# Kernel tuning notes

Measured on AMD Instinct MI355X. Metric: run time of the kernel, lower is better.

Reference implementation:

```python
import jax, jax.numpy as jnp
import numpy as np

B, NT, NZ, NX, NREC = 4, 256, 192, 192, 128
DT, DH = 0.001, 10.0


def setup_inputs() -> dict:
    key = jax.random.key(0)
    k1, k2, k3, k4 = jax.random.split(key, 4)
    # source wavelets, one trace per shot
    x = jax.random.normal(k1, (B, NT, 1), dtype=jnp.float32) * 1e2
    # realistic elastic media
    vp = 2500.0 + 1000.0 * jax.random.uniform(k2, (NZ, NX), dtype=jnp.float32)
    vs = vp / 1.78
    rho = 2000.0 + 300.0 * jax.random.uniform(k3, (NZ, NX), dtype=jnp.float32)
    # per-shot source location (z=5 near surface, random x)
    src_x = jax.random.randint(k4, (B,), 10, NX - 10)
    src_loc = jnp.stack([jnp.full((B,), 5), src_x], axis=1).astype(jnp.int32)
    # receiver line at depth z=5
    rec_x = jnp.linspace(10, NX - 10, NREC).astype(jnp.int32)
    rec_loc = jnp.stack([jnp.full((NREC,), 5, dtype=jnp.int32), rec_x], axis=1)
    return {"x": x, "vp": vp, "vs": vs, "rho": rho,
            "src_loc": src_loc, "rec_loc": rec_loc}


# staggered-grid first differences (forward / backward), zero-padded at edges
def _dxf(f):
    return jnp.pad(jnp.diff(f, axis=-1), ((0, 0), (0, 0), (0, 1))) / DH

def _dxb(f):
    return jnp.pad(jnp.diff(f, axis=-1), ((0, 0), (0, 0), (1, 0))) / DH

def _dzf(f):
    return jnp.pad(jnp.diff(f, axis=-2), ((0, 0), (0, 1), (0, 0))) / DH

def _dzb(f):
    return jnp.pad(jnp.diff(f, axis=-2), ((0, 0), (1, 0), (0, 0))) / DH


def _propagate(x, vp, vs, rho, src_loc, rec_loc):
    lam = rho * (vp ** 2 - 2.0 * vs ** 2)
    mu = rho * vs ** 2
    lam2mu = lam + 2.0 * mu
    buoy = DT / rho  # buoyancy * dt
    bidx = jnp.arange(B)
    sz, sx = src_loc[:, 0], src_loc[:, 1]
    rz, rx = rec_loc[:, 0], rec_loc[:, 1]

    def step(carry, wav_t):
        vx, vz, txx, tzz, txz = carry
        # velocity update from stress divergence
        vx = vx + buoy * (_dxf(txx) + _dzb(txz))
        vz = vz + buoy * (_dxb(txz) + _dzf(tzz))
        # stress update from velocity gradients
        dvxdx = _dxb(vx)
        dvzdz = _dzb(vz)
        txx = txx + DT * (lam2mu * dvxdx + lam * dvzdz)
        tzz = tzz + DT * (lam * dvxdx + lam2mu * dvzdz)
        txz = txz + DT * mu * (_dzf(vx) + _dxf(vz))
        # explosive source injection into txx, tzz (source_type = ['txx','tzz'])
        txx = txx.at[bidx, sz, sx].add(wav_t)
        tzz = tzz.at[bidx, sz, sx].add(wav_t)
        # probe extraction: (B, NREC)
        return (vx, vz, txx, tzz, txz), (vx[:, rz, rx], vz[:, rz, rx])

    z = jnp.zeros((B, NZ, NX), dtype=vp.dtype)
    _, (rvx, rvz) = jax.lax.scan(step, (z, z, z, z, z), x[:, :, 0].T)
    # torch: stack(dim=1) -> (B,NT,NREC); permute(1,2,0) -> (NT,NREC,B); cat dim=2
    y_vx = jnp.transpose(rvx, (0, 2, 1))  # (NT, NREC, B)
    y_vz = jnp.transpose(rvz, (0, 2, 1))
    return jnp.concatenate([y_vx, y_vz], axis=2)  # (NT, NREC, 2B)


def reference(x, vp, vs, rho, src_loc, rec_loc):
    return _propagate(x, vp, vs, rho, src_loc, rec_loc)
```

## Files before the change

### kernel.cpp

```cpp
#include <hip/hip_runtime.h>

#pragma clang fp contract(off)

#define B_    4
#define NT_   256
#define NZ_   192
#define NX_   192
#define NREC_ 128
#define DT_   0.001f
#define DH_   10.0f

#define N_CELL  (NZ_ * NX_)
#define N_FIELD (B_ * N_CELL)

#define K_     4
#define ROWS   3
#define NTHR   1024
#define VH     (2 * K_ - 1)
#define SH     (2 * K_)
#define VROWS  (ROWS + 2 * VH)
#define SROWS  (ROWS + 2 * SH)
#define TILES  (NZ_ / ROWS)
#define NBLK   (B_ * TILES)
#define NX4    (NX_ / 4)
#define LDS_BYTES ((2 * VROWS + 3 * SROWS) * NX_ * 4)

using f4 = __attribute__((ext_vector_type(4))) float;

__device__ __forceinline__ int imax_(int a, int b) { return a > b ? a : b; }
__device__ __forceinline__ int imin_(int a, int b) { return a < b ? a : b; }

__global__ void mat_kernel(const float* __restrict__ vp, const float* __restrict__ vs,
                           const float* __restrict__ rho,
                           float* __restrict__ lam, float* __restrict__ dtmu,
                           float* __restrict__ lam2mu, float* __restrict__ buoy) {
    int i = blockIdx.x * blockDim.x + threadIdx.x;
    if (i >= N_CELL) return;
    float vpi = vp[i], vsi = vs[i], rhoi = rho[i];
    float vs2 = vsi * vsi;
    float mui = rhoi * vs2;
    float lami = rhoi * (vpi * vpi - 2.0f * vs2);
    lam[i] = lami;
    dtmu[i] = DT_ * mui;
    lam2mu[i] = lami + 2.0f * mui;
    buoy[i] = DT_ / rhoi;
}

template<int S>
__device__ __forceinline__ void substep(
    int tid, int z0, int base, int zv0, int zs0, int sz, int sx, int b, int t0,
    float* __restrict__ vxl, float* __restrict__ vzl,
    float* __restrict__ txxl, float* __restrict__ tzzl, float* __restrict__ txzl,
    const float* __restrict__ lam, const float* __restrict__ dtmu,
    const float* __restrict__ l2m, const float* __restrict__ buoy,
    const float* __restrict__ wav,
    bool rec_ok, int rec_idx, float* __restrict__ out,
    float* __restrict__ vxw, float* __restrict__ vzw,
    float* __restrict__ txxw, float* __restrict__ tzzw, float* __restrict__ txzw) {
    const int t = t0 + S;

    {
        constexpr int hv = 2 * (K_ - 1 - S) + 1;
        const int zlo = imax_(0, z0 - hv);
        const int zhi = imin_(NZ_ - 1, z0 + ROWS - 1 + hv);
        const int n4  = (zhi - zlo + 1) * NX4;
        if (tid < n4) {
            int dz = tid / NX4;
            int x4 = tid - dz * NX4;
            int z  = zlo + dz;
            int x0 = x4 * 4;
            int zsrow = (z - zs0) * NX_;
            int zvrow = (z - zv0) * NX_;
            const f4* txxR = reinterpret_cast<const f4*>(txxl + zsrow);
            const f4* txzR = reinterpret_cast<const f4*>(txzl + zsrow);
            const f4* txzM = reinterpret_cast<const f4*>(txzl + zsrow - NX_);
            const f4* tzzR = reinterpret_cast<const f4*>(tzzl + zsrow);
            const f4* tzzP = reinterpret_cast<const f4*>(tzzl + zsrow + NX_);
            f4 txo  = txxR[x4];
            f4 txn  = txxR[x4 < NX4 - 1 ? x4 + 1 : x4];
            f4 tzo  = txzR[x4];
            f4 tzp  = txzR[x4 > 0 ? x4 - 1 : x4];
            f4 tzm  = txzM[x4];
            f4 tzzo = tzzR[x4];
            f4 tzzp = tzzP[x4];
            f4 vxo  = reinterpret_cast<const f4*>(vxl + zvrow)[x4];
            f4 vzo  = reinterpret_cast<const f4*>(vzl + zvrow)[x4];
            f4 bu   = *reinterpret_cast<const f4*>(buoy + z * NX_ + x0);
            f4 nvx, nvz;
#pragma unroll
            for (int e = 0; e < 4; ++e) {
                int xg = x0 + e;
                float txx_c = txo[e];
                float txxp1 = (e == 3) ? txn[0] : txo[e + 1];
                float txz_c = tzo[e];
                float txzm1 = (e == 0) ? tzp[3] : tzo[e - 1];
                float dxf_txx = (xg < NX_ - 1) ? (txxp1 - txx_c) / DH_ : 0.0f;
                float dzb_txz = (z >= 1)       ? (txz_c - tzm[e]) / DH_ : 0.0f;
                float dxb_txz = (xg >= 1)      ? (txz_c - txzm1) / DH_ : 0.0f;
                float dzf_tzz = (z < NZ_ - 1)  ? (tzzp[e] - tzzo[e]) / DH_ : 0.0f;
                nvx[e] = vxo[e] + bu[e] * (dxf_txx + dzb_txz);
                nvz[e] = vzo[e] + bu[e] * (dxb_txz + dzf_tzz);
            }
            reinterpret_cast<f4*>(vxl + zvrow)[x4] = nvx;
            reinterpret_cast<f4*>(vzl + zvrow)[x4] = nvz;
            if (S == K_ - 1) {
                if (z >= z0 && z < z0 + ROWS) {
                    *reinterpret_cast<f4*>(vxw + base + z * NX_ + x0) = nvx;
                    *reinterpret_cast<f4*>(vzw + base + z * NX_ + x0) = nvz;
                }
            }
        }
    }
    __syncthreads();

    if (rec_ok) {
        size_t o = ((size_t)t * NREC_ + tid) * (2 * B_);
        out[o + b]      = vxl[rec_idx];
        out[o + B_ + b] = vzl[rec_idx];
    }

    {
        constexpr int hs = 2 * (K_ - 1 - S);
        const int zlo = imax_(0, z0 - hs);
        const int zhi = imin_(NZ_ - 1, z0 + ROWS - 1 + hs);
        const int n4  = (zhi - zlo + 1) * NX4;
        if (tid < n4) {
            int dz = tid / NX4;
            int x4 = tid - dz * NX4;
            int z  = zlo + dz;
            int x0 = x4 * 4;
            int zsrow = (z - zs0) * NX_;
            int zvrow = (z - zv0) * NX_;
            const f4* vxR = reinterpret_cast<const f4*>(vxl + zvrow);
            const f4* vxP = reinterpret_cast<const f4*>(vxl + zvrow + NX_);
            const f4* vzR = reinterpret_cast<const f4*>(vzl + zvrow);
            const f4* vzM = reinterpret_cast<const f4*>(vzl + zvrow - NX_);
            f4 vxo  = vxR[x4];
            f4 vxp  = vxR[x4 > 0 ? x4 - 1 : x4];
            f4 vxzp = vxP[x4];
            f4 vzo  = vzR[x4];
            f4 vzn  = vzR[x4 < NX4 - 1 ? x4 + 1 : x4];
            f4 vzm  = vzM[x4];
            f4 txxo = reinterpret_cast<const f4*>(txxl + zsrow)[x4];
            f4 tzzo = reinterpret_cast<const f4*>(tzzl + zsrow)[x4];
            f4 txzo = reinterpret_cast<const f4*>(txzl + zsrow)[x4];
            int c0 = z * NX_ + x0;
            f4 l   = *reinterpret_cast<const f4*>(lam  + c0);
            f4 lm  = *reinterpret_cast<const f4*>(l2m  + c0);
            f4 dtm = *reinterpret_cast<const f4*>(dtmu + c0);
            float w = wav[b * NT_ + t];
            f4 ntxx, ntzz, ntxz;
#pragma unroll
            for (int e = 0; e < 4; ++e) {
                int xg = x0 + e;
                float vx_c = vxo[e];
                float vz_c = vzo[e];
                float vxm1 = (e == 0) ? vxp[3] : vxo[e - 1];
                float vzp1 = (e == 3) ? vzn[0] : vzo[e + 1];
                float dvxdx  = (xg >= 1)      ? (vx_c - vxm1) / DH_ : 0.0f;
                float dvzdz  = (z >= 1)       ? (vz_c - vzm[e]) / DH_ : 0.0f;
                float dzf_vx = (z < NZ_ - 1)  ? (vxzp[e] - vx_c) / DH_ : 0.0f;
                float dxf_vz = (xg < NX_ - 1) ? (vzp1 - vz_c) / DH_ : 0.0f;
                float a  = txxo[e] + DT_ * (lm[e] * dvxdx + l[e] * dvzdz);
                float bb = tzzo[e] + DT_ * (l[e] * dvxdx + lm[e] * dvzdz);
                float cc = txzo[e] + dtm[e] * (dzf_vx + dxf_vz);
                if (z == sz && xg == sx) { a = a + w; bb = bb + w; }
                ntxx[e] = a; ntzz[e] = bb; ntxz[e] = cc;
            }
            reinterpret_cast<f4*>(txxl + zsrow)[x4] = ntxx;
            reinterpret_cast<f4*>(tzzl + zsrow)[x4] = ntzz;
            reinterpret_cast<f4*>(txzl + zsrow)[x4] = ntxz;
            if (S == K_ - 1) {
                *reinterpret_cast<f4*>(txxw + base + c0) = ntxx;
                *reinterpret_cast<f4*>(tzzw + base + c0) = ntzz;
                *reinterpret_cast<f4*>(txzw + base + c0) = ntxz;
            }
        }
    }
    __syncthreads();
}

__global__ void __launch_bounds__(NTHR, 4)
step_kernel(const float* __restrict__ vxr, const float* __restrict__ vzr,
            const float* __restrict__ txxr, const float* __restrict__ tzzr,
            const float* __restrict__ txzr,
            float* __restrict__ vxw, float* __restrict__ vzw,
            float* __restrict__ txxw, float* __restrict__ tzzw, float* __restrict__ txzw,
            const float* __restrict__ lam, const float* __restrict__ dtmu,
            const float* __restrict__ l2m, const float* __restrict__ buoy,
            const float* __restrict__ wav, int t0,
            const int* __restrict__ src_loc, const int* __restrict__ rec_loc,
            float* __restrict__ out) {
    extern __shared__ float smem[];
    float* __restrict__ vxl  = smem;
    float* __restrict__ vzl  = vxl  + VROWS * NX_;
    float* __restrict__ txxl = vzl  + VROWS * NX_;
    float* __restrict__ tzzl = txxl + SROWS * NX_;
    float* __restrict__ txzl = tzzl + SROWS * NX_;

    const int tid  = threadIdx.x;
    const int b    = blockIdx.x / TILES;
    const int tile = blockIdx.x % TILES;
    const int z0   = tile * ROWS;
    const int base = b * N_CELL;
    const int zv0  = z0 - VH;
    const int zs0  = z0 - SH;

    const int sz = src_loc[2 * b];
    const int sx = src_loc[2 * b + 1];

    bool rec_ok = false;
    int rec_idx = 0;
    if (tid < NREC_) {
        int rz = rec_loc[2 * tid];
        int rx = rec_loc[2 * tid + 1];
        if (rz >= z0 && rz < z0 + ROWS) {
            rec_ok = true;
            rec_idx = (rz - zv0) * NX_ + rx;
        }
    }

    if (tid < SROWS * NX4) {
        int dz = tid / NX4;
        int x4 = tid - dz * NX4;
        int z  = zs0 + dz;
        if (z >= 0 && z < NZ_) {
            int g = base + z * NX_ + x4 * 4;
            reinterpret_cast<f4*>(txxl)[tid] = *reinterpret_cast<const f4*>(txxr + g);
            reinterpret_cast<f4*>(tzzl)[tid] = *reinterpret_cast<const f4*>(tzzr + g);
            reinterpret_cast<f4*>(txzl)[tid] = *reinterpret_cast<const f4*>(txzr + g);
        }
    }
    if (tid < VROWS * NX4) {
        int dz = tid / NX4;
        int x4 = tid - dz * NX4;
        int z  = zv0 + dz;
        if (z >= 0 && z < NZ_) {
            int g = base + z * NX_ + x4 * 4;
            reinterpret_cast<f4*>(vxl)[tid] = *reinterpret_cast<const f4*>(vxr + g);
            reinterpret_cast<f4*>(vzl)[tid] = *reinterpret_cast<const f4*>(vzr + g);
        }
    }
    __syncthreads();

    substep<0>(tid, z0, base, zv0, zs0, sz, sx, b, t0, vxl, vzl, txxl, tzzl, txzl,
               lam, dtmu, l2m, buoy, wav, rec_ok, rec_idx, out, vxw, vzw, txxw, tzzw, txzw);
    substep<1>(tid, z0, base, zv0, zs0, sz, sx, b, t0, vxl, vzl, txxl, tzzl, txzl,
               lam, dtmu, l2m, buoy, wav, rec_ok, rec_idx, out, vxw, vzw, txxw, tzzw, txzw);
    substep<2>(tid, z0, base, zv0, zs0, sz, sx, b, t0, vxl, vzl, txxl, tzzl, txzl,
               lam, dtmu, l2m, buoy, wav, rec_ok, rec_idx, out, vxw, vzw, txxw, tzzw, txzw);
    substep<3>(tid, z0, base, zv0, zs0, sz, sx, b, t0, vxl, vzl, txxl, tzzl, txzl,
               lam, dtmu, l2m, buoy, wav, rec_ok, rec_idx, out, vxw, vzw, txxw, tzzw, txzw);
}

extern "C" void kernel_launch(void* const* d_in, const int* in_sizes, int n_in,
                              void* d_out, int out_size, void* d_ws, size_t ws_size,
                              hipStream_t stream) {
    const float* xw      = (const float*)d_in[0];
    const float* vp      = (const float*)d_in[1];
    const float* vs      = (const float*)d_in[2];
    const float* rho     = (const float*)d_in[3];
    const int*   src_loc = (const int*)d_in[4];
    const int*   rec_loc = (const int*)d_in[5];
    float*       out     = (float*)d_out;

    float* ws = (float*)d_ws;
    float* vx[2]  = { ws + 0 * N_FIELD, ws + 1 * N_FIELD };
    float* vz[2]  = { ws + 2 * N_FIELD, ws + 3 * N_FIELD };
    float* txx[2] = { ws + 4 * N_FIELD, ws + 5 * N_FIELD };
    float* tzz[2] = { ws + 6 * N_FIELD, ws + 7 * N_FIELD };
    float* txz[2] = { ws + 8 * N_FIELD, ws + 9 * N_FIELD };
    float* lam    = ws + 10 * N_FIELD;
    float* dtmu   = lam + N_CELL;
    float* l2m    = dtmu + N_CELL;
    float* buoy   = l2m + N_CELL;

    hipMemsetAsync(d_ws, 0, (size_t)10 * N_FIELD * sizeof(float), stream);

    mat_kernel<<<(N_CELL + 255) / 256, 256, 0, stream>>>(vp, vs, rho, lam, dtmu, l2m, buoy);

    for (int L = 0; L < NT_ / K_; ++L) {
        int p = L & 1;
        step_kernel<<<NBLK, NTHR, LDS_BYTES, stream>>>(
            vx[p], vz[p], txx[p], tzz[p], txz[p],
            vx[1 - p], vz[1 - p], txx[1 - p], tzz[1 - p], txz[1 - p],
            lam, dtmu, l2m, buoy,
            xw, L * K_, src_loc, rec_loc, out);
    }
}
```

Before: 1.198 ms.

## Deepen temporal blocking to eight steps, load first substep from global, remap XCDs

Raises temporal blocking from four to eight time steps per launch, which halves the number of kernel launches and global round-trips while enlarging the redundant halo recomputation (the halo now exceeds the thread count, so the work is looped). The separate global-to-LDS prologue is removed: substep 0 reads its stencil inputs straight from global memory, and the LDS stress halo shrinks accordingly. Block indices are remapped across 8 XCDs so neighbouring tiles share an L2, and the occupancy hint in the launch bounds is dropped. The cost is more LDS per block, more halo compute and fewer resident blocks.

```diff
diff --git a/kernel.cpp b/kernel.cpp
--- a/kernel.cpp
+++ b/kernel.cpp
@@ -13,22 +13,25 @@
 #define N_CELL  (NZ_ * NX_)
 #define N_FIELD (B_ * N_CELL)
 
-#define K_     4
+#define K_     8
 #define ROWS   3
 #define NTHR   1024
 #define VH     (2 * K_ - 1)
-#define SH     (2 * K_)
+#define HS0    (2 * (K_ - 1))
 #define VROWS  (ROWS + 2 * VH)
-#define SROWS  (ROWS + 2 * SH)
+#define SROWSL (ROWS + 2 * HS0)
 #define TILES  (NZ_ / ROWS)
 #define NBLK   (B_ * TILES)
 #define NX4    (NX_ / 4)
-#define LDS_BYTES ((2 * VROWS + 3 * SROWS) * NX_ * 4)
+#define NXCD   8
+#define LDS_BYTES ((2 * VROWS + 3 * SROWSL) * NX_ * 4)
 
 using f4 = __attribute__((ext_vector_type(4))) float;
 
 __device__ __forceinline__ int imax_(int a, int b) { return a > b ? a : b; }
 __device__ __forceinline__ int imin_(int a, int b) { return a < b ? a : b; }
+__device__ __forceinline__ f4 LD4(const float* p) { return *reinterpret_cast<const f4*>(p); }
+__device__ __forceinline__ void ST4(float* p, f4 v) { *reinterpret_cast<f4*>(p) = v; }
 
 __global__ void mat_kernel(const float* __restrict__ vp, const float* __restrict__ vs,
                            const float* __restrict__ rho,
@@ -51,6 +54,9 @@
     int tid, int z0, int base, int zv0, int zs0, int sz, int sx, int b, int t0,
     float* __restrict__ vxl, float* __restrict__ vzl,
     float* __restrict__ txxl, float* __restrict__ tzzl, float* __restrict__ txzl,
+    const float* __restrict__ vxr, const float* __restrict__ vzr,
+    const float* __restrict__ txxr, const float* __restrict__ tzzr,
+    const float* __restrict__ txzr,
     const float* __restrict__ lam, const float* __restrict__ dtmu,
     const float* __restrict__ l2m, const float* __restrict__ buoy,
     const float* __restrict__ wav,
@@ -60,53 +66,71 @@
     const int t = t0 + S;
 
     {
-        constexpr int hv = 2 * (K_ - 1 - S) + 1;
+        constexpr int hv   = 2 * (K_ - 1 - S) + 1;
+        constexpr int MAXR = ROWS + 2 * hv;
+        constexpr int ITER = (MAXR * NX4 + NTHR - 1) / NTHR;
         const int zlo = imax_(0, z0 - hv);
         const int zhi = imin_(NZ_ - 1, z0 + ROWS - 1 + hv);
         const int n4  = (zhi - zlo + 1) * NX4;
-        if (tid < n4) {
-            int dz = tid / NX4;
-            int x4 = tid - dz * NX4;
-            int z  = zlo + dz;
-            int x0 = x4 * 4;
-            int zsrow = (z - zs0) * NX_;
-            int zvrow = (z - zv0) * NX_;
-            const f4* txxR = reinterpret_cast<const f4*>(txxl + zsrow);
-            const f4* txzR = reinterpret_cast<const f4*>(txzl + zsrow);
-            const f4* txzM = reinterpret_cast<const f4*>(txzl + zsrow - NX_);
-            const f4* tzzR = reinterpret_cast<const f4*>(tzzl + zsrow);
-            const f4* tzzP = reinterpret_cast<const f4*>(tzzl + zsrow + NX_);
-            f4 txo  = txxR[x4];
-            f4 txn  = txxR[x4 < NX4 - 1 ? x4 + 1 : x4];
-            f4 tzo  = txzR[x4];
-            f4 tzp  = txzR[x4 > 0 ? x4 - 1 : x4];
-            f4 tzm  = txzM[x4];
-            f4 tzzo = tzzR[x4];
-            f4 tzzp = tzzP[x4];
-            f4 vxo  = reinterpret_cast<const f4*>(vxl + zvrow)[x4];
-            f4 vzo  = reinterpret_cast<const f4*>(vzl + zvrow)[x4];
-            f4 bu   = *reinterpret_cast<const f4*>(buoy + z * NX_ + x0);
-            f4 nvx, nvz;
 #pragma unroll
-            for (int e = 0; e < 4; ++e) {
-                int xg = x0 + e;
-                float txx_c = txo[e];
-                float txxp1 = (e == 3) ? txn[0] : txo[e + 1];
-                float txz_c = tzo[e];
-                float txzm1 = (e == 0) ? tzp[3] : tzo[e - 1];
-                float dxf_txx = (xg < NX_ - 1) ? (txxp1 - txx_c) / DH_ : 0.0f;
-                float dzb_txz = (z >= 1)       ? (txz_c - tzm[e]) / DH_ : 0.0f;
-                float dxb_txz = (xg >= 1)      ? (txz_c - txzm1) / DH_ : 0.0f;
-                float dzf_tzz = (z < NZ_ - 1)  ? (tzzp[e] - tzzo[e]) / DH_ : 0.0f;
-                nvx[e] = vxo[e] + bu[e] * (dxf_txx + dzb_txz);
-                nvz[e] = vzo[e] + bu[e] * (dxb_txz + dzf_tzz);
-            }
-            reinterpret_cast<f4*>(vxl + zvrow)[x4] = nvx;
-            reinterpret_cast<f4*>(vzl + zvrow)[x4] = nvz;
-            if (S == K_ - 1) {
-                if (z >= z0 && z < z0 + ROWS) {
-                    *reinterpret_cast<f4*>(vxw + base + z * NX_ + x0) = nvx;
-                    *reinterpret_cast<f4*>(vzw + base + z * NX_ + x0) = nvz;
+        for (int it = 0; it < ITER; ++it) {
+            int idx = tid + it * NTHR;
+            if (idx < n4) {
+                int dz  = idx / NX4;
+                int x4i = idx - dz * NX4;
+                int x0i = x4i * 4;
+                int z   = zlo + dz;
+                f4 txo, txn, tzo, tzp, tzm, tzzo, tzzp, vxo, vzo;
+                if (S == 0) {
+                    int gz  = base + z * NX_ + x0i;
+                    int gzm = base + imax_(z - 1, 0) * NX_ + x0i;
+                    int gzp = base + imin_(z + 1, NZ_ - 1) * NX_ + x0i;
+                    txo  = LD4(txxr + gz);
+                    txn  = LD4(txxr + gz + (x4i < NX4 - 1 ? 4 : 0));
+                    tzo  = LD4(txzr + gz);
+                    tzp  = LD4(txzr + gz - (x4i > 0 ? 4 : 0));
+                    tzm  = LD4(txzr + gzm);
+                    tzzo = LD4(tzzr + gz);
+                    tzzp = LD4(tzzr + gzp);
+                    vxo  = LD4(vxr + gz);
+                    vzo  = LD4(vzr + gz);
+                } else {
+                    int sOff = (z - zs0) * NX_ + x0i;
+                    int vOff = (z - zv0) * NX_ + x0i;
+                    txo  = LD4(txxl + sOff);
+                    txn  = LD4(txxl + sOff + (x4i < NX4 - 1 ? 4 : 0));
+                    tzo  = LD4(txzl + sOff);
+                    tzp  = LD4(txzl + sOff - (x4i > 0 ? 4 : 0));
+                    tzm  = LD4(txzl + sOff - NX_);
+                    tzzo = LD4(tzzl + sOff);
+                    tzzp = LD4(tzzl + sOff + NX_);
+                    vxo  = LD4(vxl + vOff);
+                    vzo  = LD4(vzl + vOff);
+                }
+                f4 bu = LD4(buoy + z * NX_ + x0i);
+                f4 nvx, nvz;
+#pragma unroll
+                for (int e = 0; e < 4; ++e) {
+                    int xg = x0i + e;
+                    float txx_c = txo[e];
+                    float txxp1 = (e == 3) ? txn[0] : txo[e + 1];
+                    float txz_c = tzo[e];
+                    float txzm1 = (e == 0) ? tzp[3] : tzo[e - 1];
+                    float dxf_txx = (xg < NX_ - 1) ? (txxp1 - txx_c) / DH_ : 0.0f;
+                    float dzb_txz = (z >= 1)       ? (txz_c - tzm[e]) / DH_ : 0.0f;
+                    float dxb_txz = (xg >= 1)      ? (txz_c - txzm1) / DH_ : 0.0f;
+                    float dzf_tzz = (z < NZ_ - 1)  ? (tzzp[e] - tzzo[e]) / DH_ : 0.0f;
+                    nvx[e] = vxo[e] + bu[e] * (dxf_txx + dzb_txz);
+                    nvz[e] = vzo[e] + bu[e] * (dxb_txz + dzf_tzz);
+                }
+                int vOff = (z - zv0) * NX_ + x0i;
+                ST4(vxl + vOff, nvx);
+                ST4(vzl + vOff, nvz);
+                if (S == K_ - 1) {
+                    if (z >= z0 && z < z0 + ROWS) {
+                        ST4(vxw + base + z * NX_ + x0i, nvx);
+                        ST4(vzw + base + z * NX_ + x0i, nvz);
+                    }
                 }
             }
         }
@@ -120,67 +144,79 @@
     }
 
     {
-        constexpr int hs = 2 * (K_ - 1 - S);
+        constexpr int hs   = 2 * (K_ - 1 - S);
+        constexpr int MAXR = ROWS + 2 * hs;
+        constexpr int ITER = (MAXR * NX4 + NTHR - 1) / NTHR;
         const int zlo = imax_(0, z0 - hs);
         const int zhi = imin_(NZ_ - 1, z0 + ROWS - 1 + hs);
         const int n4  = (zhi - zlo + 1) * NX4;
-        if (tid < n4) {
-            int dz = tid / NX4;
-            int x4 = tid - dz * NX4;
-            int z  = zlo + dz;
-            int x0 = x4 * 4;
-            int zsrow = (z - zs0) * NX_;
-            int zvrow = (z - zv0) * NX_;
-            const f4* vxR = reinterpret_cast<const f4*>(vxl + zvrow);
-            const f4* vxP = reinterpret_cast<const f4*>(vxl + zvrow + NX_);
-            const f4* vzR = reinterpret_cast<const f4*>(vzl + zvrow);
-            const f4* vzM = reinterpret_cast<const f4*>(vzl + zvrow - NX_);
-            f4 vxo  = vxR[x4];
-            f4 vxp  = vxR[x4 > 0 ? x4 - 1 : x4];
-            f4 vxzp = vxP[x4];
-            f4 vzo  = vzR[x4];
-            f4 vzn  = vzR[x4 < NX4 - 1 ? x4 + 1 : x4];
-            f4 vzm  = vzM[x4];
-            f4 txxo = reinterpret_cast<const f4*>(txxl + zsrow)[x4];
-            f4 tzzo = reinterpret_cast<const f4*>(tzzl + zsrow)[x4];
-            f4 txzo = reinterpret_cast<const f4*>(txzl + zsrow)[x4];
-            int c0 = z * NX_ + x0;
-            f4 l   = *reinterpret_cast<const f4*>(lam  + c0);
-            f4 lm  = *reinterpret_cast<const f4*>(l2m  + c0);
-            f4 dtm = *reinterpret_cast<const f4*>(dtmu + c0);
-            float w = wav[b * NT_ + t];
-            f4 ntxx, ntzz, ntxz;
 #pragma unroll
-            for (int e = 0; e < 4; ++e) {
-                int xg = x0 + e;
-                float vx_c = vxo[e];
-                float vz_c = vzo[e];
-                float vxm1 = (e == 0) ? vxp[3] : vxo[e - 1];
-                float vzp1 = (e == 3) ? vzn[0] : vzo[e + 1];
-                float dvxdx  = (xg >= 1)      ? (vx_c - vxm1) / DH_ : 0.0f;
-                float dvzdz  = (z >= 1)       ? (vz_c - vzm[e]) / DH_ : 0.0f;
-                float dzf_vx = (z < NZ_ - 1)  ? (vxzp[e] - vx_c) / DH_ : 0.0f;
-                float dxf_vz = (xg < NX_ - 1) ? (vzp1 - vz_c) / DH_ : 0.0f;
-                float a  = txxo[e] + DT_ * (lm[e] * dvxdx + l[e] * dvzdz);
-                float bb = tzzo[e] + DT_ * (l[e] * dvxdx + lm[e] * dvzdz);
-                float cc = txzo[e] + dtm[e] * (dzf_vx + dxf_vz);
-                if (z == sz && xg == sx) { a = a + w; bb = bb + w; }
-                ntxx[e] = a; ntzz[e] = bb; ntxz[e] = cc;
-            }
-            reinterpret_cast<f4*>(txxl + zsrow)[x4] = ntxx;
-            reinterpret_cast<f4*>(tzzl + zsrow)[x4] = ntzz;
-            reinterpret_cast<f4*>(txzl + zsrow)[x4] = ntxz;
-            if (S == K_ - 1) {
-                *reinterpret_cast<f4*>(txxw + base + c0) = ntxx;
-                *reinterpret_cast<f4*>(tzzw + base + c0) = ntzz;
-                *reinterpret_cast<f4*>(txzw + base + c0) = ntxz;
+        for (int it = 0; it < ITER; ++it) {
+            int idx = tid + it * NTHR;
+            if (idx < n4) {
+                int dz  = idx / NX4;
+                int x4i = idx - dz * NX4;
+                int x0i = x4i * 4;
+                int z   = zlo + dz;
+                int vOff = (z - zv0) * NX_ + x0i;
+                f4 vxo  = LD4(vxl + vOff);
+                f4 vxp  = LD4(vxl + vOff - (x4i > 0 ? 4 : 0));
+                f4 vxzp = LD4(vxl + vOff + NX_);
+                f4 vzo  = LD4(vzl + vOff);
+                f4 vzn  = LD4(vzl + vOff + (x4i < NX4 - 1 ? 4 : 0));
+                f4 vzm  = LD4(vzl + vOff - NX_);
+                f4 txxo, tzzo, txzo;
+                if (S == 0) {
+                    int gz = base + z * NX_ + x0i;
+                    txxo = LD4(txxr + gz);
+                    tzzo = LD4(tzzr + gz);
+                    txzo = LD4(txzr + gz);
+                } else {
+                    int sOff = (z - zs0) * NX_ + x0i;
+                    txxo = LD4(txxl + sOff);
+                    tzzo = LD4(tzzl + sOff);
+                    txzo = LD4(txzl + sOff);
+                }
+                int c0 = z * NX_ + x0i;
+                f4 l   = LD4(lam  + c0);
+                f4 lm  = LD4(l2m  + c0);
+                f4 dtm = LD4(dtmu + c0);
+                float w = wav[b * NT_ + t];
+                f4 ntxx, ntzz, ntxz;
+#pragma unroll
+                for (int e = 0; e < 4; ++e) {
+                    int xg = x0i + e;
+                    float vx_c = vxo[e];
+                    float vz_c = vzo[e];
+                    float vxm1 = (e == 0) ? vxp[3] : vxo[e - 1];
+                    float vzp1 = (e == 3) ? vzn[0] : vzo[e + 1];
+                    float dvxdx  = (xg >= 1)      ? (vx_c - vxm1) / DH_ : 0.0f;
+                    float dvzdz  = (z >= 1)       ? (vz_c - vzm[e]) / DH_ : 0.0f;
+                    float dzf_vx = (z < NZ_ - 1)  ? (vxzp[e] - vx_c) / DH_ : 0.0f;
+                    float dxf_vz = (xg < NX_ - 1) ? (vzp1 - vz_c) / DH_ : 0.0f;
+                    float a  = txxo[e] + DT_ * (lm[e] * dvxdx + l[e] * dvzdz);
+                    float bb = tzzo[e] + DT_ * (l[e] * dvxdx + lm[e] * dvzdz);
+                    float cc = txzo[e] + dtm[e] * (dzf_vx + dxf_vz);
+                    if (z == sz && xg == sx) { a = a + w; bb = bb + w; }
+                    ntxx[e] = a; ntzz[e] = bb; ntxz[e] = cc;
+                }
+                int sOff = (z - zs0) * NX_ + x0i;
+                ST4(txxl + sOff, ntxx);
+                ST4(tzzl + sOff, ntzz);
+                ST4(txzl + sOff, ntxz);
+                if (S == K_ - 1) {
+                    int g = base + c0;
+                    ST4(txxw + g, ntxx);
+                    ST4(tzzw + g, ntzz);
+                    ST4(txzw + g, ntxz);
+                }
             }
         }
     }
     __syncthreads();
 }
 
-__global__ void __launch_bounds__(NTHR, 4)
+__global__ void __launch_bounds__(NTHR)
 step_kernel(const float* __restrict__ vxr, const float* __restrict__ vzr,
             const float* __restrict__ txxr, const float* __restrict__ tzzr,
             const float* __restrict__ txzr,
@@ -195,16 +231,17 @@
     float* __restrict__ vxl  = smem;
     float* __restrict__ vzl  = vxl  + VROWS * NX_;
     float* __restrict__ txxl = vzl  + VROWS * NX_;
-    float* __restrict__ tzzl = txxl + SROWS * NX_;
-    float* __restrict__ txzl = tzzl + SROWS * NX_;
+    float* __restrict__ tzzl = txxl + SROWSL * NX_;
+    float* __restrict__ txzl = tzzl + SROWSL * NX_;
 
     const int tid  = threadIdx.x;
-    const int b    = blockIdx.x / TILES;
-    const int tile = blockIdx.x % TILES;
+    const int wg   = (blockIdx.x % NXCD) * (NBLK / NXCD) + blockIdx.x / NXCD;
+    const int b    = wg / TILES;
+    const int tile = wg % TILES;
     const int z0   = tile * ROWS;
     const int base = b * N_CELL;
     const int zv0  = z0 - VH;
-    const int zs0  = z0 - SH;
+    const int zs0  = z0 - HS0;
 
     const int sz = src_loc[2 * b];
     const int sx = src_loc[2 * b + 1];
@@ -220,37 +257,30 @@
         }
     }
 
-    if (tid < SROWS * NX4) {
-        int dz = tid / NX4;
-        int x4 = tid - dz * NX4;
-        int z  = zs0 + dz;
-        if (z >= 0 && z < NZ_) {
-            int g = base + z * NX_ + x4 * 4;
-            reinterpret_cast<f4*>(txxl)[tid] = *reinterpret_cast<const f4*>(txxr + g);
-            reinterpret_cast<f4*>(tzzl)[tid] = *reinterpret_cast<const f4*>(tzzr + g);
-            reinterpret_cast<f4*>(txzl)[tid] = *reinterpret_cast<const f4*>(txzr + g);
-        }
-    }
-    if (tid < VROWS * NX4) {
-        int dz = tid / NX4;
-        int x4 = tid - dz * NX4;
-        int z  = zv0 + dz;
-        if (z >= 0 && z < NZ_) {
-            int g = base + z * NX_ + x4 * 4;
-            reinterpret_cast<f4*>(vxl)[tid] = *reinterpret_cast<const f4*>(vxr + g);
-            reinterpret_cast<f4*>(vzl)[tid] = *reinterpret_cast<const f4*>(vzr + g);
-        }
-    }
-    __syncthreads();
-
     substep<0>(tid, z0, base, zv0, zs0, sz, sx, b, t0, vxl, vzl, txxl, tzzl, txzl,
-               lam, dtmu, l2m, buoy, wav, rec_ok, rec_idx, out, vxw, vzw, txxw, tzzw, txzw);
+               vxr, vzr, txxr, tzzr, txzr, lam, dtmu, l2m, buoy, wav,
+               rec_ok, rec_idx, out, vxw, vzw, txxw, tzzw, txzw);
     substep<1>(tid, z0, base, zv0, zs0, sz, sx, b, t0, vxl, vzl, txxl, tzzl, txzl,
-               lam, dtmu, l2m, buoy, wav, rec_ok, rec_idx, out, vxw, vzw, txxw, tzzw, txzw);
+               vxr, vzr, txxr, tzzr, txzr, lam, dtmu, l2m, buoy, wav,
+               rec_ok, rec_idx, out, vxw, vzw, txxw, tzzw, txzw);
     substep<2>(tid, z0, base, zv0, zs0, sz, sx, b, t0, vxl, vzl, txxl, tzzl, txzl,
-               lam, dtmu, l2m, buoy, wav, rec_ok, rec_idx, out, vxw, vzw, txxw, tzzw, txzw);
+               vxr, vzr, txxr, tzzr, txzr, lam, dtmu, l2m, buoy, wav,
+               rec_ok, rec_idx, out, vxw, vzw, txxw, tzzw, txzw);
     substep<3>(tid, z0, base, zv0, zs0, sz, sx, b, t0, vxl, vzl, txxl, tzzl, txzl,
-               lam, dtmu, l2m, buoy, wav, rec_ok, rec_idx, out, vxw, vzw, txxw, tzzw, txzw);
+               vxr, vzr, txxr, tzzr, txzr, lam, dtmu, l2m, buoy, wav,
+               rec_ok, rec_idx, out, vxw, vzw, txxw, tzzw, txzw);
+    substep<4>(tid, z0, base, zv0, zs0, sz, sx, b, t0, vxl, vzl, txxl, tzzl, txzl,
+               vxr, vzr, txxr, tzzr, txzr, lam, dtmu, l2m, buoy, wav,
+               rec_ok, rec_idx, out, vxw, vzw, txxw, tzzw, txzw);
+    substep<5>(tid, z0, base, zv0, zs0, sz, sx, b, t0, vxl, vzl, txxl, tzzl, txzl,
+               vxr, vzr, txxr, tzzr, txzr, lam, dtmu, l2m, buoy, wav,
+               rec_ok, rec_idx, out, vxw, vzw, txxw, tzzw, txzw);
+    substep<6>(tid, z0, base, zv0, zs0, sz, sx, b, t0, vxl, vzl, txxl, tzzl, txzl,
+               vxr, vzr, txxr, tzzr, txzr, lam, dtmu, l2m, buoy, wav,
+               rec_ok, rec_idx, out, vxw, vzw, txxw, tzzw, txzw);
+    substep<7>(tid, z0, base, zv0, zs0, sz, sx, b, t0, vxl, vzl, txxl, tzzl, txzl,
+               vxr, vzr, txxr, tzzr, txzr, lam, dtmu, l2m, buoy, wav,
+               rec_ok, rec_idx, out, vxw, vzw, txxw, tzzw, txzw);
 }
 
 extern "C" void kernel_launch(void* const* d_in, const int* in_sizes, int n_in,
```

New measurement: 1.166 ms. -2.7%, faster.
